# Kernel optimization log

Measured on AMD Instinct MI355X. Metric: run time of the kernel, lower is better.

Reference implementation:

```python
import jax, jax.numpy as jnp
import numpy as np

HS, WS = 64, 64
SIGMA = 1.2
UPDATE_COEFF = 0.2
R = 3
N_BLOCKS = 3
GROUPS = 8
EPS_GN = 1e-5
CM, CP, CS, CT, HID = 64, 3, 128, 128, 128
B, T, HIN, WIN = 32, 256, 128, 128


def setup_inputs() -> dict:
    key = jax.random.key(0)
    ks = jax.random.split(key, 10)
    s = 0.02
    cin = CM + CP + CT
    f32 = jnp.float32
    return {
        'M': jax.random.normal(ks[0], (B, CM, HIN, WIN), f32),
        'x0_hat_norm': jax.random.uniform(ks[1], (B, T, 2), f32, -1.0, 1.0),
        't_embed': jax.random.normal(ks[2], (B, CT), f32),
        'in_proj_w': jax.random.normal(ks[3], (CS, cin), f32) * s,
        'in_proj_b': jnp.zeros((CS,), f32),
        'rb_c1w': jax.random.normal(ks[4], (N_BLOCKS, CS, CS, 3, 3), f32) * s,
        'rb_c1b': jnp.zeros((N_BLOCKS, CS), f32),
        'rb_g1w': jnp.ones((N_BLOCKS, CS), f32),
        'rb_g1b': jnp.zeros((N_BLOCKS, CS), f32),
        'rb_c2w': jax.random.normal(ks[5], (N_BLOCKS, CS, CS, 3, 3), f32) * s,
        'rb_c2b': jnp.zeros((N_BLOCKS, CS), f32),
        'rb_g2w': jnp.ones((N_BLOCKS, CS), f32),
        'rb_g2b': jnp.zeros((N_BLOCKS, CS), f32),
        'out_w': jax.random.normal(ks[6], (CS, CS), f32) * s,
        'out_b': jnp.zeros((CS,), f32),
        'mlp_w1': jax.random.normal(ks[7], (CS + CT, HID), f32) * s,
        'mlp_b1': jnp.zeros((HID,), f32),
        'mlp_w2': jax.random.normal(ks[8], (HID, HID), f32) * s,
        'mlp_b2': jnp.zeros((HID,), f32),
        'mlp_w3': jax.random.normal(ks[9], (HID, 2), f32) * s,
        'mlp_b3': jnp.zeros((2,), f32),
    }


def _resize_bilinear(M, Hs, Ws):
    # torch F.interpolate bilinear, align_corners=False, no antialias
    Bn, C, H, W = M.shape
    def coords(n_out, n_in):
        sc = n_in / n_out
        c = (jnp.arange(n_out, dtype=M.dtype) + 0.5) * sc - 0.5
        c = jnp.clip(c, 0.0, n_in - 1.0)
        i0 = jnp.floor(c)
        f = c - i0
        i0 = i0.astype(jnp.int32)
        i1 = jnp.minimum(i0 + 1, n_in - 1)
        return i0, i1, f
    y0, y1, fy = coords(Hs, H)
    x0, x1, fx = coords(Ws, W)
    top = M[:, :, y0, :] * (1 - fy)[None, None, :, None] + M[:, :, y1, :] * fy[None, None, :, None]
    return top[:, :, :, x0] * (1 - fx)[None, None, None, :] + top[:, :, :, x1] * fx[None, None, None, :]


def _rasterize_vel(pts, H, W, sigma):
    # pts: (B,T,2) pixel coords -> (B,3,H,W) [heat, vx, vy]
    xs = jnp.arange(W, dtype=pts.dtype)
    ys = jnp.arange(H, dtype=pts.dtype)
    d2 = (pts[:, :, None, None, 0] - xs[None, None, None, :]) ** 2 \
       + (pts[:, :, None, None, 1] - ys[None, None, :, None]) ** 2  # (B,T,H,W)
    w = jnp.exp(-0.5 * d2 / (sigma ** 2 + 1e-8))
    heat = w.max(axis=1)
    v = jnp.pad(jnp.diff(pts, axis=1), ((0, 0), (1, 0), (0, 0)))
    vx = (w * v[:, :, None, None, 0]).sum(axis=1)
    vy = (w * v[:, :, None, None, 1]).sum(axis=1)
    wsum = jnp.maximum(w.sum(axis=1), 1e-6)
    return jnp.stack([heat, vx / wsum, vy / wsum], axis=1)


def _conv3x3(x, w, b):
    y = jax.lax.conv_general_dilated(x, w, (1, 1), 'SAME', dimension_numbers=('NCHW', 'OIHW', 'NCHW'))
    return y + b[None, :, None, None]


def _gn(x, g, b):
    Bn, C, H, W = x.shape
    xr = x.reshape(Bn, GROUPS, C // GROUPS, H, W)
    mu = xr.mean(axis=(2, 3, 4), keepdims=True)
    var = xr.var(axis=(2, 3, 4), keepdims=True)
    xn = ((xr - mu) * jax.lax.rsqrt(var + EPS_GN)).reshape(Bn, C, H, W)
    return xn * g[None, :, None, None] + b[None, :, None, None]


def _grid_sample(S, coords):
    # bilinear, align_corners=False, zero padding. coords (B,T,2) in [-1,1] -> (B,T,C)
    Bn, C, H, W = S.shape
    Tn = coords.shape[1]
    x = ((coords[..., 0] + 1.0) * W - 1.0) * 0.5
    y = ((coords[..., 1] + 1.0) * H - 1.0) * 0.5
    x0 = jnp.floor(x)
    y0 = jnp.floor(y)
    wx = x - x0
    wy = y - y0
    Sf = S.reshape(Bn, C, H * W)
    out = jnp.zeros((Bn, C, Tn), S.dtype)
    for xi, yi, wgt in ((x0, y0, (1 - wx) * (1 - wy)), (x0 + 1, y0, wx * (1 - wy)),
                        (x0, y0 + 1, (1 - wx) * wy), (x0 + 1, y0 + 1, wx * wy)):
        valid = (xi >= 0) & (xi <= W - 1) & (yi >= 0) & (yi <= H - 1)
        xc = jnp.clip(xi, 0, W - 1).astype(jnp.int32)
        yc = jnp.clip(yi, 0, H - 1).astype(jnp.int32)
        idx = jnp.broadcast_to((yc * W + xc)[:, None, :], (Bn, C, Tn))
        g = jnp.take_along_axis(Sf, idx, axis=2)
        out = out + g * (wgt * valid)[:, None, :]
    return out.transpose(0, 2, 1)


def _forward(M, x0_hat_norm, t_embed, in_proj_w, in_proj_b, rb_c1w, rb_c1b, rb_g1w, rb_g1b,
             rb_c2w, rb_c2b, rb_g2w, rb_g2b, out_w, out_b,
             mlp_w1, mlp_b1, mlp_w2, mlp_b2, mlp_w3, mlp_b3):
    Bn = M.shape[0]
    Ms = _resize_bilinear(M, HS, WS)
    t_map = jnp.broadcast_to(t_embed[:, :, None, None], (Bn, CT, HS, WS))
    x = x0_hat_norm
    for _ in range(R):
        x_pix = jnp.stack([(x[..., 0] + 1) * 0.5 * (WS - 1), (x[..., 1] + 1) * 0.5 * (HS - 1)], axis=-1)
        P = _rasterize_vel(x_pix, HS, WS, SIGMA)  # (B,3,HS,WS)
        # SpatialRefine
        inp = jnp.concatenate([Ms, P, t_map], axis=1)
        S = jnp.einsum('bihw,oi->bohw', inp, in_proj_w) + in_proj_b[None, :, None, None]
        for i in range(N_BLOCKS):
            h = jax.nn.silu(_gn(_conv3x3(S, rb_c1w[i], rb_c1b[i]), rb_g1w[i], rb_g1b[i]))
            h = _gn(_conv3x3(h, rb_c2w[i], rb_c2b[i]), rb_g2w[i], rb_g2b[i])
            S = jax.nn.silu(S + h)
        S = jnp.einsum('bihw,oi->bohw', S, out_w) + out_b[None, :, None, None]
        # PointCorrector
        read = _grid_sample(S, x)  # (B,T,CS)
        t_tok = jnp.broadcast_to(t_embed[:, None, :], (Bn, read.shape[1], CT))
        feat = jnp.concatenate([read, t_tok], axis=-1)
        h = jax.nn.silu(feat @ mlp_w1 + mlp_b1)
        h = jax.nn.silu(h @ mlp_w2 + mlp_b2)
        dx = h @ mlp_w3 + mlp_b3
        x = jnp.clip(x + UPDATE_COEFF * dx, -1.0, 1.0)
    return x


def reference(M, x0_hat_norm, t_embed, in_proj_w, in_proj_b, rb_c1w, rb_c1b, rb_g1w, rb_g1b,
              rb_c2w, rb_c2b, rb_g2w, rb_g2b, out_w, out_b,
              mlp_w1, mlp_b1, mlp_w2, mlp_b2, mlp_w3, mlp_b3):
    return _forward(M, x0_hat_norm, t_embed, in_proj_w, in_proj_b, rb_c1w, rb_c1b, rb_g1w, rb_g1b,
                    rb_c2w, rb_c2b, rb_g2w, rb_g2b, out_w, out_b,
                    mlp_w1, mlp_b1, mlp_w2, mlp_b2, mlp_w3, mlp_b3)
```

## Files before the change

### kernel.cpp

```cpp
#include <hip/hip_runtime.h>
#include <cstddef>

#define BN 32
#define TN 256
#define PW 68
#define PLANE 4488

typedef __attribute__((ext_vector_type(8))) short bf16x8;
typedef __attribute__((ext_vector_type(4))) float f32x4;

struct __attribute__((aligned(16))) U4 { unsigned x, y, z, w; };

__device__ __forceinline__ float silu_f(float v) { return v / (1.f + __expf(-v)); }

__device__ __forceinline__ unsigned short f2bf(float f) {
  unsigned u = __float_as_uint(f);
  unsigned r = (u + 0x7fffu + ((u >> 16) & 1u)) >> 16;
  return (unsigned short)r;
}
__device__ __forceinline__ float bf2f(unsigned short h) {
  return __uint_as_float((unsigned)h << 16);
}
__device__ __forceinline__ unsigned pack2(float a, float b) {
  return (unsigned)f2bf(a) | ((unsigned)f2bf(b) << 16);
}

__device__ __forceinline__ void gld16(const unsigned short* g, unsigned short* l) {
  __builtin_amdgcn_global_load_lds((const __attribute__((address_space(1))) unsigned int*)g,
                                   (__attribute__((address_space(3))) unsigned int*)l, 16, 0, 0);
}

__global__ __launch_bounds__(256) void copy_kernel(const float* __restrict__ src, float* __restrict__ dst, int n) {
  int i = blockIdx.x * 256 + threadIdx.x;
  if (i < n) dst[i] = src[i];
}

__global__ __launch_bounds__(256) void zstats_kernel(float* __restrict__ s) {
  int i = blockIdx.x * 256 + threadIdx.x;
  if (i < 18 * 512) s[i] = 0.f;
}

__global__ __launch_bounds__(256) void zerohalo_kernel(unsigned short* __restrict__ base) {
  int idx = blockIdx.x * 256 + threadIdx.x;
  if (idx >= 384 * 1568) return;
  int p = idx / 1568, rem = idx % 1568;
  int hp = rem >> 2, icq = rem & 3;
  int row, x;
  if (hp < 68) { row = 0; x = hp; }
  else if (hp < 136) { row = 65; x = hp - 68; }
  else {
    int i = hp - 136;
    row = 1 + (i >> 2);
    const int cols[4] = {0, 1, 66, 67};
    x = cols[i & 3];
  }
  U4 z = {0u, 0u, 0u, 0u};
  *(U4*)&base[((size_t)p * PLANE + row * PW + x) * 32 + icq * 8] = z;
}

__global__ __launch_bounds__(256) void resize_t_kernel(const float* __restrict__ M, unsigned short* __restrict__ Ms4) {
  __shared__ unsigned short lt[4 * 64 * 72];
  int b = blockIdx.y, yt = blockIdx.x;
  int tid = threadIdx.x;
  for (int i = tid; i < 4 * 64 * 64; i += 256) {
    int c = i >> 8, y = (i >> 6) & 3, x = i & 63;
    const float* p = M + (((size_t)(b * 64 + c) * 128) + (yt * 4 + y) * 2) * 128 + 2 * x;
    float2 a = *(const float2*)p;
    float2 bq = *(const float2*)(p + 128);
    lt[(y * 64 + x) * 72 + c] = f2bf(0.25f * (a.x + a.y + bq.x + bq.y));
  }
  __syncthreads();
  for (int i = tid; i < 2048; i += 256) {
    int icq = i & 3, pxl = (i >> 2) & 255, cc = i >> 10;
    U4 q = *(const U4*)&lt[pxl * 72 + cc * 32 + icq * 8];
    int y = yt * 4 + (pxl >> 6), x = pxl & 63;
    *(U4*)&Ms4[(((size_t)(b * 2 + cc) * PLANE) + (size_t)(y + 1) * PW + x + 2) * 32 + icq * 8] = q;
  }
}

__global__ __launch_bounds__(256) void wprep_kernel(const float* __restrict__ Wsrc, unsigned short* __restrict__ Wdst) {
  int idx = blockIdx.x * 256 + threadIdx.x;
  if (idx >= 147456) return;
  int icp = idx & 31;
  int oc = (idx >> 5) & 127;
  int tc = idx >> 12;
  int t = tc >> 2, cch = tc & 3;
  Wdst[idx] = f2bf(Wsrc[(size_t)oc * 1152 + (size_t)(cch * 32 + icp) * 9 + t]);
}

__global__ __launch_bounds__(256) void wprep_in_kernel(const float* __restrict__ ipw, unsigned short* __restrict__ wi) {
  int idx = blockIdx.x * 256 + threadIdx.x;
  if (idx >= 12288) return;
  int icp = idx & 31, oc = (idx >> 5) & 127, cc = idx >> 12;
  float f = 0.f;
  if (cc < 2) f = ipw[oc * 195 + cc * 32 + icp];
  else if (icp < 3) f = ipw[oc * 195 + 64 + icp];
  wi[idx] = f2bf(f);
}

__global__ __launch_bounds__(256) void wprep_out_kernel(const float* __restrict__ ow, unsigned short* __restrict__ wo) {
  int idx = blockIdx.x * 256 + threadIdx.x;
  if (idx >= 16384) return;
  int icp = idx & 31, oc = (idx >> 5) & 127, cc = idx >> 12;
  wo[idx] = f2bf(ow[oc * 128 + cc * 32 + icp]);
}

__global__ __launch_bounds__(256) void tctr_kernel(const float* __restrict__ w, const float* __restrict__ bias,
                                                   const float* __restrict__ te, float* __restrict__ tctr) {
  int i = blockIdx.x * 256 + threadIdx.x;
  if (i >= BN * 128) return;
  int b = i >> 7, o = i & 127;
  float acc = bias[o];
  const float* wp = w + (size_t)o * 195 + 67;
  const float* t = te + b * 128;
  #pragma unroll 8
  for (int k = 0; k < 128; ++k) acc += wp[k] * t[k];
  tctr[i] = acc;
}

__global__ __launch_bounds__(256) void tpart_kernel(const float* __restrict__ w1, const float* __restrict__ b1,
                                                    const float* __restrict__ te, float* __restrict__ tp) {
  int i = blockIdx.x * 256 + threadIdx.x;
  if (i >= BN * 128) return;
  int b = i >> 7, j = i & 127;
  float acc = b1[j];
  #pragma unroll 8
  for (int k = 0; k < 128; ++k) acc += te[b * 128 + k] * w1[(size_t)(128 + k) * 128 + j];
  tp[i] = acc;
}

__global__ __launch_bounds__(256) void raster4_kernel(const float* __restrict__ x, unsigned short* __restrict__ Pp) {
  int b = blockIdx.y, blk = blockIdx.x;
  int tid = threadIdx.x;
  int pix = blk * 256 + tid;
  __shared__ float spx[TN], spy[TN];
  __shared__ unsigned short lp[256 * 32];
  spx[tid] = (x[(b * TN + tid) * 2] + 1.f) * 0.5f * 63.f;
  spy[tid] = (x[(b * TN + tid) * 2 + 1] + 1.f) * 0.5f * 63.f;
  __syncthreads();
  float fx = (float)(pix & 63), fy = (float)(pix >> 6);
  const float coef = -0.5f / (1.44f + 1e-8f);
  float heat = 0.f, sx = 0.f, sy = 0.f, sw = 0.f;
  float prevx = 0.f, prevy = 0.f;
  for (int t = 0; t < TN; ++t) {
    float px = spx[t], py = spy[t];
    float ddx = px - fx, ddy = py - fy;
    float w = __expf(coef * (ddx * ddx + ddy * ddy));
    heat = fmaxf(heat, w);
    float vx = (t == 0) ? 0.f : px - prevx;
    float vy = (t == 0) ? 0.f : py - prevy;
    prevx = px; prevy = py;
    sx += w * vx; sy += w * vy; sw += w;
  }
  float inv = 1.f / fmaxf(sw, 1e-6f);
  U4 q0; q0.x = pack2(heat, sx * inv); q0.y = pack2(sy * inv, 0.f); q0.z = 0u; q0.w = 0u;
  U4 z = {0u, 0u, 0u, 0u};
  *(U4*)&lp[tid * 32 + 0] = q0;
  *(U4*)&lp[tid * 32 + 8] = z;
  *(U4*)&lp[tid * 32 + 16] = z;
  *(U4*)&lp[tid * 32 + 24] = z;
  __syncthreads();
  for (int it = 0; it < 4; ++it) {
    int sid = it * 256 + tid;
    int pxl = sid >> 2, icq = sid & 3;
    int gp = blk * 256 + pxl;
    int y = gp >> 6, xx = gp & 63;
    *(U4*)&Pp[((size_t)b * PLANE + (size_t)(y + 1) * PW + xx + 2) * 32 + icq * 8] = *(const U4*)&lp[pxl * 32 + icq * 8];
  }
}

__global__ __launch_bounds__(512, 4) void conv3_v6(const unsigned short* __restrict__ In4,
                                                   const unsigned short* __restrict__ Wb,
                                                   const float* __restrict__ Bias,
                                                   float* __restrict__ stOut,
                                                   unsigned short* __restrict__ Out4) {
  __shared__ unsigned short lds[2][13056];
  __shared__ float sred[8][4][2];
  const int P = blockIdx.x;
  const int L = (P & 7) * 64 + (P >> 3);
  const int b = L >> 4, y0 = (L & 15) * 4;
  const int tid = threadIdx.x, l = tid & 63, w = tid >> 6;
  const int ocg = w & 1, rowg = w >> 1, l15 = l & 15, k8 = l >> 4;

  f32x4 acc[4][4];
  #pragma unroll
  for (int mf = 0; mf < 4; ++mf)
    #pragma unroll
    for (int nf = 0; nf < 4; ++nf) acc[mf][nf] = (f32x4){0.f, 0.f, 0.f, 0.f};

  auto issue_stage = [&](int cc, int nb) {
    const unsigned short* slab = In4 + (((size_t)(b * 4 + cc)) * PLANE + (size_t)y0 * PW) * 32;
    #pragma unroll
    for (int i = 0; i < 3; ++i) {
      int G = i * 512 + tid;
      int q = G >> 2;
      int r = q / 68;
      int xs = q - r * 68;
      int src = (G & ~3) | ((G & 3) ^ ((xs >> 1) & 3));
      gld16(slab + (size_t)src * 8, &lds[nb][(size_t)(i * 512 + w * 64) * 8]);
    }
    if (tid < 96) {
      int G = 1536 + tid;
      int q = G >> 2;
      int r = q / 68;
      int xs = q - r * 68;
      int src = (G & ~3) | ((G & 3) ^ ((xs >> 1) & 3));
      gld16(slab + (size_t)src * 8, &lds[nb][(size_t)(1536 + w * 64) * 8]);
    }
  };

  issue_stage(0, 0);
  __syncthreads();

  for (int cc = 0; cc < 4; ++cc) {
    const unsigned short* cur = &lds[cc & 1][0];
    if (cc < 3) issue_stage(cc + 1, (cc & 1) ^ 1);
    #pragma unroll
    for (int t = 0; t < 9; ++t) {
      const int ky = t / 3, kx = t - ky * 3;
      bf16x8 a[4];
      #pragma unroll
      for (int mf = 0; mf < 4; ++mf)
        a[mf] = *(const bf16x8*)&Wb[(((size_t)(t * 4 + cc) * 128) + ocg * 64 + mf * 16 + l15) * 32 + k8 * 8];
      #pragma unroll
      for (int nf = 0; nf < 4; ++nf) {
        int col = nf * 16 + l15 + kx + 1;
        int slot = ((rowg + ky) * 68 + col) * 4 + (k8 ^ ((col >> 1) & 3));
        bf16x8 bv = *(const bf16x8*)&cur[(size_t)slot * 8];
        #pragma unroll
        for (int mf = 0; mf < 4; ++mf)
          acc[mf][nf] = __builtin_amdgcn_mfma_f32_16x16x32_bf16(a[mf], bv, acc[mf][nf], 0, 0, 0);
      }
    }
    __syncthreads();
  }

  #pragma unroll
  for (int mf = 0; mf < 4; ++mf) {
    int oc = ocg * 64 + mf * 16 + k8 * 4;
    float4 bv4 = *(const float4*)&Bias[oc];
    float s = 0.f, qq = 0.f;
    #pragma unroll
    for (int nf = 0; nf < 4; ++nf) {
      float v0 = acc[mf][nf][0] + bv4.x;
      float v1 = acc[mf][nf][1] + bv4.y;
      float v2 = acc[mf][nf][2] + bv4.z;
      float v3 = acc[mf][nf][3] + bv4.w;
      s += (v0 + v1) + (v2 + v3);
      qq += (v0 * v0 + v1 * v1) + (v2 * v2 + v3 * v3);
    }
    #pragma unroll
    for (int off = 32; off > 0; off >>= 1) {
      s += __shfl_xor(s, off, 64);
      qq += __shfl_xor(qq, off, 64);
    }
    if (l == 0) { sred[w][mf][0] = s; sred[w][mf][1] = qq; }
  }
  __syncthreads();
  if (tid < 8) {
    int g = tid, og = g >> 2, mf = g & 3;
    float s = (sred[og][mf][0] + sred[og + 2][mf][0]) + (sred[og + 4][mf][0] + sred[og + 6][mf][0]);
    float qq = (sred[og][mf][1] + sred[og + 2][mf][1]) + (sred[og + 4][mf][1] + sred[og + 6][mf][1]);
    atomicAdd(&stOut[(b * 8 + g) * 2], s);
    atomicAdd(&stOut[(b * 8 + g) * 2 + 1], qq);
  }

  unsigned short* eb = &lds[0][0];
  #pragma unroll
  for (int h = 0; h < 2; ++h) {
    if ((rowg >> 1) == h) {
      int prow = rowg & 1;
      #pragma unroll
      for (int mf = 0; mf < 4; ++mf) {
        int oc = ocg * 64 + mf * 16 + k8 * 4;
        float4 bv4 = *(const float4*)&Bias[oc];
        #pragma unroll
        for (int nf = 0; nf < 4; ++nf) {
          int pxl = prow * 64 + nf * 16 + l15;
          unsigned lo = pack2(acc[mf][nf][0] + bv4.x, acc[mf][nf][1] + bv4.y);
          unsigned hi = pack2(acc[mf][nf][2] + bv4.z, acc[mf][nf][3] + bv4.w);
          unsigned off = (unsigned)(pxl * 256 + oc * 2) ^ ((pxl & 7) << 4);
          *(uint2*)((char*)eb + off) = make_uint2(lo, hi);
        }
      }
    }
    __syncthreads();
    {
      int pxl = tid >> 2, icq = tid & 3;
      int px = h * 128 + pxl;
      int yy = px >> 6, xx = px & 63;
      #pragma unroll
      for (int cc2 = 0; cc2 < 4; ++cc2) {
        unsigned off = (unsigned)(pxl * 256 + cc2 * 64 + icq * 16) ^ ((pxl & 7) << 4);
        U4 q = *(const U4*)((char*)eb + off);
        *(U4*)&Out4[(((size_t)(b * 4 + cc2)) * PLANE + (size_t)(y0 + yy + 1) * PW + xx + 2) * 32 + icq * 8] = q;
      }
    }
    __syncthreads();
  }
}

__global__ __launch_bounds__(256, 2) void conv1_v2(const unsigned short* __restrict__ srcA, int ncA,
                                                   const unsigned short* __restrict__ srcB, int nc,
                                                   const unsigned short* __restrict__ Wb,
                                                   const float* __restrict__ Bias, int perB,
                                                   unsigned short* __restrict__ Out4) {
  __shared__ unsigned short lds[32768];
  const int P = blockIdx.x;
  const int L = (P & 7) * 64 + (P >> 3);
  const int b = L >> 4, px0 = (L & 15) * 256;
  const int tid = threadIdx.x, l = tid & 63, w = tid >> 6;
  const int ocg = w & 1, rowg = w >> 1, l15 = l & 15, k8 = l >> 4;

  f32x4 acc[4][8];
  #pragma unroll
  for (int mf = 0; mf < 4; ++mf)
    #pragma unroll
    for (int nf = 0; nf < 8; ++nf) acc[mf][nf] = (f32x4){0.f, 0.f, 0.f, 0.f};

  for (int cc = 0; cc < nc; ++cc) {
    const unsigned short* base = (cc < ncA) ? srcA + ((size_t)(b * ncA + cc)) * PLANE * 32
                                            : srcB + ((size_t)b) * PLANE * 32;
    bf16x8 a[4];
    #pragma unroll
    for (int mf = 0; mf < 4; ++mf)
      a[mf] = *(const bf16x8*)&Wb[(((size_t)cc * 128) + ocg * 64 + mf * 16 + l15) * 32 + k8 * 8];
    #pragma unroll
    for (int nf = 0; nf < 8; ++nf) {
      int px = px0 + rowg * 128 + nf * 16 + l15;
      int y = px >> 6, x = px & 63;
      bf16x8 bv = *(const bf16x8*)&base[((size_t)(y + 1) * PW + x + 2) * 32 + k8 * 8];
      #pragma unroll
      for (int mf = 0; mf < 4; ++mf)
        acc[mf][nf] = __builtin_amdgcn_mfma_f32_16x16x32_bf16(a[mf], bv, acc[mf][nf], 0, 0, 0);
    }
  }
  const float* bp = Bias + (perB ? b * 128 : 0);
  #pragma unroll
  for (int mf = 0; mf < 4; ++mf) {
    int oc = ocg * 64 + mf * 16 + k8 * 4;
    float4 bv4 = *(const float4*)&bp[oc];
    #pragma unroll
    for (int nf = 0; nf < 8; ++nf) {
      int pxl = rowg * 128 + nf * 16 + l15;
      unsigned lo = pack2(acc[mf][nf][0] + bv4.x, acc[mf][nf][1] + bv4.y);
      unsigned hi = pack2(acc[mf][nf][2] + bv4.z, acc[mf][nf][3] + bv4.w);
      unsigned off = (unsigned)(pxl * 256 + oc * 2) ^ ((pxl & 7) << 4);
      *(uint2*)((char*)lds + off) = make_uint2(lo, hi);
    }
  }
  __syncthreads();
  #pragma unroll
  for (int cc2 = 0; cc2 < 4; ++cc2)
    #pragma unroll
    for (int it = 0; it < 4; ++it) {
      int sid = it * 256 + tid;
      int pxl = sid >> 2, icq = sid & 3;
      unsigned off = (unsigned)(pxl * 256 + cc2 * 64 + icq * 16) ^ ((pxl & 7) << 4);
      U4 q = *(const U4*)((char*)lds + off);
      int px = px0 + pxl;
      int yy = px >> 6, xx = px & 63;
      *(U4*)&Out4[(((size_t)(b * 4 + cc2)) * PLANE + (size_t)(yy + 1) * PW + xx + 2) * 32 + icq * 8] = q;
    }
}

__global__ __launch_bounds__(256) void gn1apply_kernel(unsigned short* __restrict__ A,
                                                       const float* __restrict__ st, const float* __restrict__ gam,
                                                       const float* __restrict__ bet) {
  size_t e8 = (size_t)blockIdx.x * 256 + threadIdx.x;
  int icq = (int)(e8 & 3), x = (int)((e8 >> 2) & 63), y = (int)((e8 >> 8) & 63);
  int cc = (int)((e8 >> 14) & 3), b = (int)(e8 >> 16);
  size_t off = (((size_t)(b * 4 + cc)) * PLANE + (size_t)(y + 1) * PW + x + 2) * 32 + icq * 8;
  int ch = icq * 8;
  int g = cc * 2 + (ch >> 4);
  const float invn = 1.f / 65536.f;
  float ssum = st[(b * 8 + g) * 2], qsum = st[(b * 8 + g) * 2 + 1];
  float mu = ssum * invn;
  float ri = rsqrtf(qsum * invn - mu * mu + 1e-5f);
  int c0 = cc * 32 + ch;
  float4 g0 = *(const float4*)&gam[c0], g1 = *(const float4*)&gam[c0 + 4];
  float4 b0 = *(const float4*)&bet[c0], b1 = *(const float4*)&bet[c0 + 4];
  float gv[8] = {g0.x, g0.y, g0.z, g0.w, g1.x, g1.y, g1.z, g1.w};
  float bv[8] = {b0.x, b0.y, b0.z, b0.w, b1.x, b1.y, b1.z, b1.w};
  U4 va = *(const U4*)&A[off];
  unsigned aa[4] = {va.x, va.y, va.z, va.w};
  unsigned out[4];
  #pragma unroll
  for (int p = 0; p < 4; ++p) {
    float h0 = (bf2f((unsigned short)(aa[p] & 0xffffu)) - mu) * ri * gv[2 * p] + bv[2 * p];
    float h1 = (bf2f((unsigned short)(aa[p] >> 16)) - mu) * ri * gv[2 * p + 1] + bv[2 * p + 1];
    out[p] = pack2(silu_f(h0), silu_f(h1));
  }
  U4 q; q.x = out[0]; q.y = out[1]; q.z = out[2]; q.w = out[3];
  *(U4*)&A[off] = q;
}

__global__ __launch_bounds__(256) void gn2add4_kernel(unsigned short* __restrict__ S, const unsigned short* __restrict__ Bb,
                                                      const float* __restrict__ st, const float* __restrict__ gam,
                                                      const float* __restrict__ bet) {
  size_t e8 = (size_t)blockIdx.x * 256 + threadIdx.x;
  int icq = (int)(e8 & 3), x = (int)((e8 >> 2) & 63), y = (int)((e8 >> 8) & 63);
  int cc = (int)((e8 >> 14) & 3), b = (int)(e8 >> 16);
  size_t off = (((size_t)(b * 4 + cc)) * PLANE + (size_t)(y + 1) * PW + x + 2) * 32 + icq * 8;
  int ch = icq * 8;
  int g = cc * 2 + (ch >> 4);
  const float invn = 1.f / 65536.f;
  float ssum = st[(b * 8 + g) * 2], qsum = st[(b * 8 + g) * 2 + 1];
  float mu = ssum * invn;
  float ri = rsqrtf(qsum * invn - mu * mu + 1e-5f);
  int c0 = cc * 32 + ch;
  float4 g0 = *(const float4*)&gam[c0], g1 = *(const float4*)&gam[c0 + 4];
  float4 b0 = *(const float4*)&bet[c0], b1 = *(const float4*)&bet[c0 + 4];
  float gv[8] = {g0.x, g0.y, g0.z, g0.w, g1.x, g1.y, g1.z, g1.w};
  float bv[8] = {b0.x, b0.y, b0.z, b0.w, b1.x, b1.y, b1.z, b1.w};
  U4 vb = *(const U4*)&Bb[off];
  U4 vs = *(const U4*)&S[off];
  unsigned ab[4] = {vb.x, vb.y, vb.z, vb.w};
  unsigned as[4] = {vs.x, vs.y, vs.z, vs.w};
  unsigned out[4];
  #pragma unroll
  for (int p = 0; p < 4; ++p) {
    float h0 = (bf2f((unsigned short)(ab[p] & 0xffffu)) - mu) * ri * gv[2 * p] + bv[2 * p];
    float h1 = (bf2f((unsigned short)(ab[p] >> 16)) - mu) * ri * gv[2 * p + 1] + bv[2 * p + 1];
    float r0 = silu_f(bf2f((unsigned short)(as[p] & 0xffffu)) + h0);
    float r1 = silu_f(bf2f((unsigned short)(as[p] >> 16)) + h1);
    out[p] = pack2(r0, r1);
  }
  U4 q; q.x = out[0]; q.y = out[1]; q.z = out[2]; q.w = out[3];
  *(U4*)&S[off] = q;
}

__global__ __launch_bounds__(128) void gsample4_kernel(const unsigned short* __restrict__ S2, const float* __restrict__ x,
                                                       float* __restrict__ rd) {
  int token = blockIdx.x, c = threadIdx.x, b = token >> 8;
  float cx = x[token * 2], cy = x[token * 2 + 1];
  float fx = (cx + 1.f) * 32.f - 0.5f;
  float fy = (cy + 1.f) * 32.f - 0.5f;
  float x0f = floorf(fx), y0f = floorf(fy);
  float wx = fx - x0f, wy = fy - y0f;
  const unsigned short* Sb = S2 + ((size_t)(b * 4 + (c >> 5)) * PLANE) * 32 + (c & 31);
  float acc = 0.f;
  #pragma unroll
  for (int cor = 0; cor < 4; ++cor) {
    float xi = x0f + (float)(cor & 1), yi = y0f + (float)(cor >> 1);
    float wgt = ((cor & 1) ? wx : 1.f - wx) * ((cor >> 1) ? wy : 1.f - wy);
    if (xi >= 0.f && xi <= 63.f && yi >= 0.f && yi <= 63.f)
      acc += bf2f(Sb[(size_t)(((int)yi + 1) * PW + (int)xi + 2) * 32]) * wgt;
  }
  rd[(size_t)token * 128 + c] = acc;
}

__global__ __launch_bounds__(256) void mlp_fc_kernel(const float* __restrict__ in, const float* __restrict__ w,
                                                     const float* __restrict__ init, int initPerB,
                                                     float* __restrict__ out) {
  int tok0 = blockIdx.x * 2;
  int tid = threadIdx.x;
  __shared__ float sr[2][128];
  sr[tid >> 7][tid & 127] = in[(size_t)tok0 * 128 + tid];
  __syncthreads();
  int t = tid >> 7, j = tid & 127;
  int token = tok0 + t;
  int b = token >> 8;
  float acc = initPerB ? init[b * 128 + j] : init[j];
  #pragma unroll 8
  for (int k = 0; k < 128; ++k) acc += sr[t][k] * w[(size_t)k * 128 + j];
  out[(size_t)token * 128 + j] = silu_f(acc);
}

__global__ __launch_bounds__(256) void mlp3_update_kernel(const float* __restrict__ h2, const float* __restrict__ w3,
                                                          const float* __restrict__ b3, float* __restrict__ x) {
  int token = blockIdx.x * 256 + threadIdx.x;
  if (token >= BN * TN) return;
  float d0 = b3[0], d1 = b3[1];
  const float* h = h2 + (size_t)token * 128;
  #pragma unroll 8
  for (int k = 0; k < 128; ++k) { float hv = h[k]; d0 += hv * w3[k * 2]; d1 += hv * w3[k * 2 + 1]; }
  float nx = x[token * 2] + 0.2f * d0;
  float ny = x[token * 2 + 1] + 0.2f * d1;
  x[token * 2] = fminf(fmaxf(nx, -1.f), 1.f);
  x[token * 2 + 1] = fminf(fmaxf(ny, -1.f), 1.f);
}

extern "C" void kernel_launch(void* const* d_in, const int* in_sizes, int n_in,
                              void* d_out, int out_size, void* d_ws, size_t ws_size,
                              hipStream_t stream) {
  const float* M   = (const float*)d_in[0];
  const float* x0  = (const float*)d_in[1];
  const float* te  = (const float*)d_in[2];
  const float* ipw = (const float*)d_in[3];
  const float* ipb = (const float*)d_in[4];
  const float* c1w = (const float*)d_in[5];
  const float* c1b = (const float*)d_in[6];
  const float* g1w = (const float*)d_in[7];
  const float* g1b = (const float*)d_in[8];
  const float* c2w = (const float*)d_in[9];
  const float* c2b = (const float*)d_in[10];
  const float* g2w = (const float*)d_in[11];
  const float* g2b = (const float*)d_in[12];
  const float* ow  = (const float*)d_in[13];
  const float* ob  = (const float*)d_in[14];
  const float* w1  = (const float*)d_in[15];
  const float* b1  = (const float*)d_in[16];
  const float* w2  = (const float*)d_in[17];
  const float* b2  = (const float*)d_in[18];
  const float* w3  = (const float*)d_in[19];
  const float* b3  = (const float*)d_in[20];

  const size_t PSH = (size_t)PLANE * 32;
  float* f     = (float*)d_ws;
  float* wx    = f;
  float* tctr  = wx + 16384;
  float* tpart = tctr + 4096;
  float* stats = tpart + 4096;
  float* rd    = stats + 9216;
  float* h1    = rd + 1048576;
  float* h2    = h1 + 1048576;
  unsigned short* S4  = (unsigned short*)(h2 + 1048576);
  unsigned short* A4  = S4 + 128 * PSH;
  unsigned short* B4  = A4 + 128 * PSH;
  unsigned short* Ms4 = B4 + 128 * PSH;
  unsigned short* Pp  = Ms4 + 64 * PSH;
  unsigned short* wc  = Pp + 32 * PSH;
  unsigned short* wi  = wc + 884736;
  unsigned short* wo  = wi + 12288;

  copy_kernel<<<64, 256, 0, stream>>>(x0, wx, 16384);
  zstats_kernel<<<36, 256, 0, stream>>>(stats);
  zerohalo_kernel<<<2352, 256, 0, stream>>>(S4);
  resize_t_kernel<<<dim3(16, 32), 256, 0, stream>>>(M, Ms4);
  tctr_kernel<<<16, 256, 0, stream>>>(ipw, ipb, te, tctr);
  tpart_kernel<<<16, 256, 0, stream>>>(w1, b1, te, tpart);
  for (int i = 0; i < 3; ++i) {
    wprep_kernel<<<576, 256, 0, stream>>>(c1w + (size_t)i * 147456, wc + (size_t)(2 * i) * 147456);
    wprep_kernel<<<576, 256, 0, stream>>>(c2w + (size_t)i * 147456, wc + (size_t)(2 * i + 1) * 147456);
  }
  wprep_in_kernel<<<48, 256, 0, stream>>>(ipw, wi);
  wprep_out_kernel<<<64, 256, 0, stream>>>(ow, wo);

  for (int r = 0; r < 3; ++r) {
    raster4_kernel<<<dim3(16, 32), 256, 0, stream>>>(wx, Pp);
    conv1_v2<<<512, 256, 0, stream>>>(Ms4, 2, Pp, 3, wi, tctr, 1, S4);
    for (int i = 0; i < 3; ++i) {
      float* stA = stats + (size_t)(r * 3 + i) * 512;
      float* stB = stats + (size_t)(9 + r * 3 + i) * 512;
      conv3_v6<<<512, 512, 0, stream>>>(S4, wc + (size_t)(2 * i) * 147456, c1b + i * 128, stA, A4);
      gn1apply_kernel<<<8192, 256, 0, stream>>>(A4, stA, g1w + i * 128, g1b + i * 128);
      conv3_v6<<<512, 512, 0, stream>>>(A4, wc + (size_t)(2 * i + 1) * 147456, c2b + i * 128, stB, B4);
      gn2add4_kernel<<<8192, 256, 0, stream>>>(S4, B4, stB, g2w + i * 128, g2b + i * 128);
    }
    conv1_v2<<<512, 256, 0, stream>>>(S4, 4, nullptr, 4, wo, ob, 0, A4);
    gsample4_kernel<<<8192, 128, 0, stream>>>(A4, wx, rd);
    mlp_fc_kernel<<<4096, 256, 0, stream>>>(rd, w1, tpart, 1, h1);
    mlp_fc_kernel<<<4096, 256, 0, stream>>>(h1, w2, b2, 0, h2);
    mlp3_update_kernel<<<32, 256, 0, stream>>>(h2, w3, b3, wx);
  }
  copy_kernel<<<64, 256, 0, stream>>>(wx, (float*)d_out, 16384);
}
```

Measured before the change: 1.788 ms.

## Fuse GroupNorm1+SiLU into second conv's LDS prologue; use nontemporal stores

Removes the standalone gn1apply pass. The second 3x3 conv now applies the first GroupNorm and SiLU to each input chunk after it lands in LDS, skipping halo slots so the zero padding stays zero. This saves a full read-modify-write of the activation buffer and one kernel launch per block. In exchange it adds a barrier and per-element transcendental work inside the conv's pipelined loop. The next stage's prefetch is also now issued after that work, so it overlaps less. Conv output stores become nontemporal.

```diff
diff --git a/kernel.cpp b/kernel.cpp
--- a/kernel.cpp
+++ b/kernel.cpp
@@ -8,6 +8,7 @@
 
 typedef __attribute__((ext_vector_type(8))) short bf16x8;
 typedef __attribute__((ext_vector_type(4))) float f32x4;
+typedef __attribute__((ext_vector_type(4))) unsigned int u32x4;
 
 struct __attribute__((aligned(16))) U4 { unsigned x, y, z, w; };
 
@@ -28,6 +29,10 @@
 __device__ __forceinline__ void gld16(const unsigned short* g, unsigned short* l) {
   __builtin_amdgcn_global_load_lds((const __attribute__((address_space(1))) unsigned int*)g,
                                    (__attribute__((address_space(3))) unsigned int*)l, 16, 0, 0);
+}
+
+__device__ __forceinline__ void nt_store16(unsigned short* p, U4 q) {
+  __builtin_nontemporal_store(__builtin_bit_cast(u32x4, q), (u32x4*)p);
 }
 
 __global__ __launch_bounds__(256) void copy_kernel(const float* __restrict__ src, float* __restrict__ dst, int n) {
@@ -169,9 +174,13 @@
   }
 }
 
-__global__ __launch_bounds__(512, 4) void conv3_v6(const unsigned short* __restrict__ In4,
+template<int FUSED>
+__global__ __launch_bounds__(512, 4) void conv3_v7(const unsigned short* __restrict__ In4,
                                                    const unsigned short* __restrict__ Wb,
                                                    const float* __restrict__ Bias,
+                                                   const float* __restrict__ stIn,
+                                                   const float* __restrict__ gam,
+                                                   const float* __restrict__ bet,
                                                    float* __restrict__ stOut,
                                                    unsigned short* __restrict__ Out4) {
   __shared__ unsigned short lds[2][13056];
@@ -181,6 +190,7 @@
   const int b = L >> 4, y0 = (L & 15) * 4;
   const int tid = threadIdx.x, l = tid & 63, w = tid >> 6;
   const int ocg = w & 1, rowg = w >> 1, l15 = l & 15, k8 = l >> 4;
+  const float invn = 1.f / 65536.f;
 
   f32x4 acc[4][4];
   #pragma unroll
@@ -213,8 +223,43 @@
   __syncthreads();
 
   for (int cc = 0; cc < 4; ++cc) {
-    const unsigned short* cur = &lds[cc & 1][0];
-    if (cc < 3) issue_stage(cc + 1, (cc & 1) ^ 1);
+    unsigned short* cur = &lds[cc & 1][0];
+    const int nb = (cc & 1) ^ 1;
+
+    if constexpr (FUSED) {
+      float s0 = stIn[(b * 8 + cc * 2) * 2], q0s = stIn[(b * 8 + cc * 2) * 2 + 1];
+      float s1 = stIn[(b * 8 + cc * 2 + 1) * 2], q1s = stIn[(b * 8 + cc * 2 + 1) * 2 + 1];
+      float mu0 = s0 * invn, ri0 = rsqrtf(q0s * invn - mu0 * mu0 + 1e-5f);
+      float mu1 = s1 * invn, ri1 = rsqrtf(q1s * invn - mu1 * mu1 + 1e-5f);
+      auto doslot = [&](int S) {
+        int q = S >> 2, r = S >> 2, xs;
+        r = q / 68; xs = q - r * 68;
+        int icq = (S & 3) ^ ((xs >> 1) & 3);
+        bool halo = (xs < 2) | (xs > 65) | ((y0 == 0) & (r == 0)) | ((y0 == 60) & (r == 5));
+        if (halo) return;
+        float mu = (icq & 2) ? mu1 : mu0;
+        float ri = (icq & 2) ? ri1 : ri0;
+        int c0 = cc * 32 + icq * 8;
+        U4 v = *(const U4*)&cur[(size_t)S * 8];
+        unsigned a[4] = {v.x, v.y, v.z, v.w};
+        unsigned o[4];
+        #pragma unroll
+        for (int p = 0; p < 4; ++p) {
+          float h0 = (bf2f((unsigned short)(a[p] & 0xffffu)) - mu) * ri * gam[c0 + 2 * p] + bet[c0 + 2 * p];
+          float h1 = (bf2f((unsigned short)(a[p] >> 16)) - mu) * ri * gam[c0 + 2 * p + 1] + bet[c0 + 2 * p + 1];
+          o[p] = pack2(silu_f(h0), silu_f(h1));
+        }
+        U4 ov; ov.x = o[0]; ov.y = o[1]; ov.z = o[2]; ov.w = o[3];
+        *(U4*)&cur[(size_t)S * 8] = ov;
+      };
+      #pragma unroll
+      for (int j = 0; j < 3; ++j) doslot(j * 512 + tid);
+      if (tid < 96) doslot(1536 + tid);
+      __syncthreads();
+    }
+
+    if (cc < 3) issue_stage(cc + 1, nb);
+
     #pragma unroll
     for (int t = 0; t < 9; ++t) {
       const int ky = t / 3, kx = t - ky * 3;
@@ -293,7 +338,7 @@
       for (int cc2 = 0; cc2 < 4; ++cc2) {
         unsigned off = (unsigned)(pxl * 256 + cc2 * 64 + icq * 16) ^ ((pxl & 7) << 4);
         U4 q = *(const U4*)((char*)eb + off);
-        *(U4*)&Out4[(((size_t)(b * 4 + cc2)) * PLANE + (size_t)(y0 + yy + 1) * PW + xx + 2) * 32 + icq * 8] = q;
+        nt_store16(&Out4[(((size_t)(b * 4 + cc2)) * PLANE + (size_t)(y0 + yy + 1) * PW + xx + 2) * 32 + icq * 8], q);
       }
     }
     __syncthreads();
@@ -362,37 +407,6 @@
       int yy = px >> 6, xx = px & 63;
       *(U4*)&Out4[(((size_t)(b * 4 + cc2)) * PLANE + (size_t)(yy + 1) * PW + xx + 2) * 32 + icq * 8] = q;
     }
-}
-
-__global__ __launch_bounds__(256) void gn1apply_kernel(unsigned short* __restrict__ A,
-                                                       const float* __restrict__ st, const float* __restrict__ gam,
-                                                       const float* __restrict__ bet) {
-  size_t e8 = (size_t)blockIdx.x * 256 + threadIdx.x;
-  int icq = (int)(e8 & 3), x = (int)((e8 >> 2) & 63), y = (int)((e8 >> 8) & 63);
-  int cc = (int)((e8 >> 14) & 3), b = (int)(e8 >> 16);
-  size_t off = (((size_t)(b * 4 + cc)) * PLANE + (size_t)(y + 1) * PW + x + 2) * 32 + icq * 8;
-  int ch = icq * 8;
-  int g = cc * 2 + (ch >> 4);
-  const float invn = 1.f / 65536.f;
-  float ssum = st[(b * 8 + g) * 2], qsum = st[(b * 8 + g) * 2 + 1];
-  float mu = ssum * invn;
-  float ri = rsqrtf(qsum * invn - mu * mu + 1e-5f);
-  int c0 = cc * 32 + ch;
-  float4 g0 = *(const float4*)&gam[c0], g1 = *(const float4*)&gam[c0 + 4];
-  float4 b0 = *(const float4*)&bet[c0], b1 = *(const float4*)&bet[c0 + 4];
-  float gv[8] = {g0.x, g0.y, g0.z, g0.w, g1.x, g1.y, g1.z, g1.w};
-  float bv[8] = {b0.x, b0.y, b0.z, b0.w, b1.x, b1.y, b1.z, b1.w};
-  U4 va = *(const U4*)&A[off];
-  unsigned aa[4] = {va.x, va.y, va.z, va.w};
-  unsigned out[4];
-  #pragma unroll
-  for (int p = 0; p < 4; ++p) {
-    float h0 = (bf2f((unsigned short)(aa[p] & 0xffffu)) - mu) * ri * gv[2 * p] + bv[2 * p];
-    float h1 = (bf2f((unsigned short)(aa[p] >> 16)) - mu) * ri * gv[2 * p + 1] + bv[2 * p + 1];
-    out[p] = pack2(silu_f(h0), silu_f(h1));
-  }
-  U4 q; q.x = out[0]; q.y = out[1]; q.z = out[2]; q.w = out[3];
-  *(U4*)&A[off] = q;
 }
 
 __global__ __launch_bounds__(256) void gn2add4_kernel(unsigned short* __restrict__ S, const unsigned short* __restrict__ Bb,
@@ -543,9 +557,10 @@
     for (int i = 0; i < 3; ++i) {
       float* stA = stats + (size_t)(r * 3 + i) * 512;
       float* stB = stats + (size_t)(9 + r * 3 + i) * 512;
-      conv3_v6<<<512, 512, 0, stream>>>(S4, wc + (size_t)(2 * i) * 147456, c1b + i * 128, stA, A4);
-      gn1apply_kernel<<<8192, 256, 0, stream>>>(A4, stA, g1w + i * 128, g1b + i * 128);
-      conv3_v6<<<512, 512, 0, stream>>>(A4, wc + (size_t)(2 * i + 1) * 147456, c2b + i * 128, stB, B4);
+      conv3_v7<0><<<512, 512, 0, stream>>>(S4, wc + (size_t)(2 * i) * 147456, c1b + i * 128,
+                                           nullptr, nullptr, nullptr, stA, A4);
+      conv3_v7<1><<<512, 512, 0, stream>>>(A4, wc + (size_t)(2 * i + 1) * 147456, c2b + i * 128,
+                                           stA, g1w + i * 128, g1b + i * 128, stB, B4);
       gn2add4_kernel<<<8192, 256, 0, stream>>>(S4, B4, stB, g2w + i * 128, g2b + i * 128);
     }
     conv1_v2<<<512, 256, 0, stream>>>(S4, 4, nullptr, 4, wo, ob, 0, A4);
```

After: 1.934 ms. +8.2%, slower.
